# Optimization experiments

Hardware: AMD Instinct MI355X
Metric: run time of the kernel (lower is better)

## Reference

```python
import jax, jax.numpy as jnp
import numpy as np

B, NTS, NOS_F, NTS_F, H, A, HIST = 8192, 64, 7, 6, 64, 9, 2


def _lstm(x, Wih, Whh, bih, bhh):
    # x: [B, T, in] -> all hidden states [B, T, H]; torch gate order (i, f, g, o)
    xg = jnp.einsum('bti,gi->btg', x, Wih) + bih + bhh  # precompute input projection
    Hh = Whh.shape[1]

    def step(carry, xt):
        h, c = carry
        gates = xt + h @ Whh.T
        i, f, g, o = jnp.split(gates, 4, axis=-1)
        c = jax.nn.sigmoid(f) * c + jax.nn.sigmoid(i) * jnp.tanh(g)
        h = jax.nn.sigmoid(o) * jnp.tanh(c)
        return (h, c), h

    z = jnp.zeros((x.shape[0], Hh), x.dtype)
    _, hs = jax.lax.scan(step, (z, z), jnp.swapaxes(xg, 0, 1))
    return jnp.swapaxes(hs, 0, 1)


def _inner(s, WOS, bOS, Wih, Whh, bih, bhh, WTS, bTS):
    # NaN-masked ragged TS sequences + dynamic last-valid-step gather
    b = s.shape[0]
    sOS = s[:, :NOS_F]
    sTS = s[:, NOS_F:].reshape(b, -1, NTS_F)
    nan = jnp.isnan(sTS)
    n = jnp.sum(~nan[:, :, 0], axis=1)          # valid TS count per row
    h_idx = jnp.maximum(n - 1, 0)
    sTS = jnp.where(nan, 0.0, sTS)
    xOS = jax.nn.relu(sOS @ WOS.T + bOS)
    hs = _lstm(sTS, Wih, Whh, bih, bhh)
    xTS = hs[jnp.arange(b), h_idx]              # hidden state at last valid step
    xTS = jax.nn.relu(xTS @ WTS.T + bTS)
    return jnp.concatenate([xOS, xTS], axis=1)  # [B, 128]


def setup_inputs() -> dict:
    key = jax.random.key(0)
    ks = iter(jax.random.split(key, 48))

    def nanify(x, k):  # NaN-pad beyond a random valid prefix length in [1, NTS]
        lens = jax.random.randint(k, x.shape[:-2], 1, NTS + 1)
        mask = jnp.arange(NTS) < lens[..., None]
        return jnp.where(mask[..., None], x, jnp.nan)

    sTS = nanify(jax.random.normal(next(ks), (B, NTS, NTS_F)), next(ks))
    s = jnp.concatenate([jax.random.normal(next(ks), (B, NOS_F)), sTS.reshape(B, -1)], axis=1)
    shTS = nanify(jax.random.normal(next(ks), (B, HIST, NTS, NTS_F)), next(ks))
    s_hist = jnp.concatenate([jax.random.normal(next(ks), (B, HIST, NOS_F)), shTS.reshape(B, HIST, -1)], axis=2)
    hist_len = jax.random.randint(next(ks), (B,), 0, HIST + 1)
    a_hist = jnp.zeros((B, HIST, 1), jnp.float32)

    p = lambda *shape: jax.random.normal(next(ks), shape, jnp.float32) * 0.1
    inp = dict(s=s, s_hist=s_hist, a_hist=a_hist, hist_len=hist_len)
    for t in (0, 1, 2):
        inp[f'WOS{t}'] = p(H, NOS_F); inp[f'bOS{t}'] = p(H)
        inp[f'Wih{t}'] = p(4 * H, NTS_F); inp[f'Whh{t}'] = p(4 * H, H)
        inp[f'bih{t}'] = p(4 * H); inp[f'bhh{t}'] = p(4 * H)
        inp[f'WTS{t}'] = p(H, H); inp[f'bTS{t}'] = p(H)
    inp['Wiho'] = p(4 * H, 2 * H); inp['Whho'] = p(4 * H, H)
    inp['biho'] = p(4 * H); inp['bhho'] = p(4 * H)
    inp['W1'] = p(H, H); inp['b1'] = p(H)
    inp['W2'] = p(A, H); inp['b2'] = p(A)
    return inp


def reference(s, s_hist, a_hist, hist_len,
              WOS0, bOS0, Wih0, Whh0, bih0, bhh0, WTS0, bTS0,
              WOS1, bOS1, Wih1, Whh1, bih1, bhh1, WTS1, bTS1,
              WOS2, bOS2, Wih2, Whh2, bih2, bhh2, WTS2, bTS2,
              Wiho, Whho, biho, bhho, W1, b1, W2, b2):
    b = s.shape[0]
    ok2 = (hist_len >= 2)[:, None]
    # torch mutates s_hist[:,0] for hist_len<2; t1_idx==0 there, so s_t1 is also zeroed
    s_t2 = jnp.where(ok2, s_hist[:, 0, :], 0.0)
    t1_idx = jnp.maximum(hist_len - 1, 0)
    s_t1 = jnp.where(ok2, s_hist[jnp.arange(b), t1_idx, :], 0.0)

    x2 = _inner(s_t2, WOS2, bOS2, Wih2, Whh2, bih2, bhh2, WTS2, bTS2)
    x1 = _inner(s_t1, WOS1, bOS1, Wih1, Whh1, bih1, bhh1, WTS1, bTS1)
    x0 = _inner(s, WOS0, bOS0, Wih0, Whh0, bih0, bhh0, WTS0, bTS0)
    x_tilde = jnp.stack([x2, x1, x0], axis=1)  # [B, 3, 128]

    # per-batch torch.roll(shift=hist_len-2): out[t] = in[(t - shift) mod L]
    L = HIST + 1
    shift = hist_len - 2
    idx = (jnp.arange(L)[None, :] - shift[:, None]) % L
    x_tilde = jnp.take_along_axis(x_tilde, idx[:, :, None], axis=1)

    hs = _lstm(x_tilde, Wiho, Whho, biho, bhho)
    hidden = hs[jnp.arange(b), hist_len]
    x = jax.nn.relu(hidden @ W1.T + b1)
    return x @ W2.T + b2
```

## Files before the change

### kernel.cpp

```cpp
#include <hip/hip_runtime.h>
#include <hip/hip_bf16.h>

#define NB 8192
#define SROW 391

#define TW      22848
#define W_WIH   0
#define W_WHH   1536
#define W_BSUM  17920
#define W_WTS   18176
#define W_BTS   22272
#define W_WOS   22336
#define W_BOS   22784
#define W_OUT   68544
#define WO_WIHO 0
#define WO_WHHO 32768
#define WO_BSUM 49152
#define WO_W1   49408
#define WO_B1   53504
#define WO_W2   53568
#define WO_B2   54144
#define WF_TOTAL 122697

#define OFF_WHH   0
#define OFF_WIH   49152
#define OFF_WTS   73728
#define OFF_WIHO  86016
#define OFF_WHHO  118784
#define OFF_W1    135168
#define FB_TOTAL  139264

typedef unsigned short u16;
typedef __attribute__((ext_vector_type(8))) short short8;
typedef __attribute__((ext_vector_type(8))) _Float16 half8;
typedef __attribute__((ext_vector_type(4))) _Float16 half4;
typedef __attribute__((ext_vector_type(4))) float float4v;

#define MFMAH(a, b, c) __builtin_amdgcn_mfma_f32_16x16x32_f16((a), (b), (c), 0, 0, 0)

__device__ __forceinline__ float bf2f(u16 u){ return __uint_as_float(((unsigned)u) << 16); }
__device__ __forceinline__ u16 f2bf(float f){
  unsigned x = __float_as_uint(f);
  unsigned r = (x + 0x7FFFu + ((x >> 16) & 1u)) >> 16;
  return (u16)r;
}
__device__ __forceinline__ u16 f2h(float f){
  _Float16 h = (_Float16)f;
  return *(u16*)&h;
}
__device__ __forceinline__ bool isnanf32(float f){
  unsigned x = __float_as_uint(f);
  return (x & 0x7FFFFFFFu) > 0x7F800000u;
}
__device__ __forceinline__ float ldin(const void* p, size_t i, bool isbf){
  if (isbf) return bf2f(((const u16*)p)[i]);
  return ((const float*)p)[i];
}
__device__ __forceinline__ float sigm(float x){ return __fdividef(1.0f, 1.0f + __expf(-x)); }
__device__ __forceinline__ float tanh_f(float x){ return __fdividef(2.0f, 1.0f + __expf(-2.0f * x)) - 1.0f; }

__device__ __forceinline__ void lstm_cell(float gi, float gf, float gg, float go,
                                          float& cs, float& hs, bool v){
  const float ef = __expf(-gf);
  const float ei = __expf(-gi);
  const float eg = __expf(-2.0f * gg);
  const float eo = __expf(-go);
  const float A = 1.0f + ef, B = 1.0f + ei, C = 1.0f + eg;
  const float BC = B * C;
  const float R = __builtin_amdgcn_rcpf(A * BC);
  const float t = fmaf(-A, eg, A);
  const float cn = fmaf(cs, BC, t) * R;
  const float ct = fminf(fmaxf(cn, -15.0f), 15.0f);
  const float ec = __expf(-2.0f * ct);
  const float D = 1.0f + eo, E = 1.0f + ec;
  const float S = __builtin_amdgcn_rcpf(D * E);
  const float hn = (1.0f - ec) * S;
  cs = v ? cn : cs;
  hs = v ? hn : hs;
}

__device__ __forceinline__ bool detect_bf(const void* whh0){
  const u16* u = (const u16*)whh0;
  const int l = threadIdx.x & 63;
  int e = (u[2 * l] >> 7) & 0xFF;
  unsigned long long m = __ballot(e >= 100 && e <= 141);
  return __popcll(m) >= 32;
}

struct Seg { int src; int src2; int soff; int dst; int n; };
struct SegTab { Seg s[35]; };
struct PtrTab { const void* p[36]; };

__global__ __launch_bounds__(256) void kweights(PtrTab P, SegTab S, float* __restrict__ WF,
                                                const void* __restrict__ whh0, int* __restrict__ flag,
                                                int* __restrict__ ghist){
  const bool isbf = detect_bf(whh0);
  if (blockIdx.x == 0){
    if (threadIdx.x == 0) *flag = isbf ? 1 : 0;
    if (threadIdx.x < 195) ghist[threadIdx.x] = 0;
  }
  Seg sg = S.s[blockIdx.x];
  const void* a = P.p[sg.src];
  const void* b = (sg.src2 >= 0) ? P.p[sg.src2] : nullptr;
  for (int i = threadIdx.x; i < sg.n; i += 256){
    float v = ldin(a, sg.soff + i, isbf);
    if (b) v += ldin(b, sg.soff + i, isbf);
    WF[sg.dst + i] = v;
  }
}

__global__ __launch_bounds__(256) void kfrag(const float* __restrict__ WF, u16* __restrict__ FB){
  const int i = blockIdx.x * 256 + threadIdx.x;
  short8 v = {0, 0, 0, 0, 0, 0, 0, 0};
  int dst;
  if (i < 6144){
    const int lane = i & 63, f = (i >> 6) & 1, g = (i >> 7) & 3, q = (i >> 9) & 3, t = i >> 11;
    const int mrow = g * 64 + q * 16 + (lane & 15);
    const float* src = WF + t * TW + W_WHH + mrow * 64 + f * 32 + (lane >> 4) * 8;
    #pragma unroll
    for (int j = 0; j < 8; ++j) v[j] = (short)f2h(src[j]);
    dst = OFF_WHH + i * 8;
  } else if (i < 9216){
    const int k = i - 6144;
    const int lane = k & 63, g = (k >> 6) & 3, q = (k >> 8) & 3, t = k >> 10;
    if ((lane >> 4) == 0){
      const int mrow = g * 64 + q * 16 + (lane & 15);
      const float* src = WF + t * TW + W_WIH + mrow * 6;
      #pragma unroll
      for (int j = 0; j < 6; ++j) v[j] = (short)f2h(src[j]);
    }
    dst = OFF_WIH + k * 8;
  } else if (i < 10752){
    const int k = i - 9216;
    const int lane = k & 63, f = (k >> 6) & 1, q = (k >> 7) & 3, t = k >> 9;
    const int row = q * 16 + (lane & 15);
    const float* src = WF + t * TW + W_WTS + row * 64 + f * 32 + (lane >> 4) * 8;
    #pragma unroll
    for (int j = 0; j < 8; ++j) v[j] = (short)f2h(src[j]);
    dst = OFF_WTS + k * 8;
  } else if (i < 14848){
    const int k = i - 10752;
    const int lane = k & 63, f = (k >> 6) & 3, g = (k >> 8) & 3, q = (k >> 10) & 3;
    const int mrow = g * 64 + q * 16 + (lane & 15);
    const float* src = WF + W_OUT + WO_WIHO + mrow * 128 + f * 32 + (lane >> 4) * 8;
    #pragma unroll
    for (int j = 0; j < 8; ++j) v[j] = (short)f2h(src[j]);
    dst = OFF_WIHO + k * 8;
  } else if (i < 16896){
    const int k = i - 14848;
    const int lane = k & 63, f = (k >> 6) & 1, g = (k >> 7) & 3, q = (k >> 9) & 3;
    const int mrow = g * 64 + q * 16 + (lane & 15);
    const float* src = WF + W_OUT + WO_WHHO + mrow * 64 + f * 32 + (lane >> 4) * 8;
    #pragma unroll
    for (int j = 0; j < 8; ++j) v[j] = (short)f2h(src[j]);
    dst = OFF_WHHO + k * 8;
  } else {
    const int k = i - 16896;
    const int lane = k & 63, f = (k >> 6) & 1, q = (k >> 7) & 3;
    const int row = q * 16 + (lane & 15);
    const float* src = WF + W_OUT + WO_W1 + row * 64 + f * 32 + (lane >> 4) * 8;
    #pragma unroll
    for (int j = 0; j < 8; ++j) v[j] = (short)f2h(src[j]);
    dst = OFF_W1 + k * 8;
  }
  *(short8*)&FB[dst] = v;
}

__global__ __launch_bounds__(256) void kprep(const void* __restrict__ s,
                                             const void* __restrict__ sh,
                                             const int* __restrict__ hist_len,
                                             const float* __restrict__ WF,
                                             u16* __restrict__ sTx,
                                             int* __restrict__ nar,
                                             u16* __restrict__ xpartT,
                                             const int* __restrict__ flag,
                                             int* __restrict__ ghist,
                                             int* __restrict__ krank){
  __shared__ u16 stage[4][400];
  const bool isbf = (*flag != 0);
  const int t = blockIdx.y;
  const int w = threadIdx.x >> 6;
  const int l = threadIdx.x & 63;
  const int b = blockIdx.x * 4 + w;
  const int hl = hist_len[b];

  const void* base; size_t soff;
  if (t == 0){ base = s; soff = (size_t)b * SROW; }
  else {
    if (hl < 2) return;
    base = sh; soff = ((size_t)b * 2 + ((t == 1) ? 1 : 0)) * SROW;
  }

  float val[7];
  #pragma unroll
  for (int k = 0; k < 7; ++k){
    const int e = k * 64 + l;
    float v = 0.0f;
    if (e < SROW) v = isbf ? bf2f(((const u16*)base)[soff + e]) : ((const float*)base)[soff + e];
    val[k] = v;
  }
  float sOS[7];
  #pragma unroll
  for (int i = 0; i < 7; ++i) sOS[i] = __shfl(val[0], i);

  int n = 0;
  #pragma unroll
  for (int k = 0; k < 7; ++k){
    const int e = k * 64 + l;
    const bool firstf = (e >= 7) && (e < SROW) && ((e - 7) % 6 == 0);
    unsigned long long m = __ballot(firstf && !isnanf32(val[k]));
    n += __popcll(m);
  }

  #pragma unroll
  for (int k = 0; k < 7; ++k){
    const int e = k * 64 + l;
    if (e >= 7 && e < SROW) stage[w][e] = f2h(isnanf32(val[k]) ? 0.0f : val[k]);
  }

  {
    const int r = l;
    u16 v0 = stage[w][7 + 6 * r],  v1 = stage[w][8 + 6 * r],  v2 = stage[w][9 + 6 * r];
    u16 v3 = stage[w][10 + 6 * r], v4 = stage[w][11 + 6 * r], v5 = stage[w][12 + 6 * r];
    uint4 wv;
    wv.x = (uint)v0 | ((uint)v1 << 16);
    wv.y = (uint)v2 | ((uint)v3 << 16);
    wv.z = (uint)v4 | ((uint)v5 << 16);
    wv.w = 0u;
    *(uint4*)&sTx[((size_t)(t * NB + b) * 64 + r) * 8] = wv;
  }
  if (l == 0){
    nar[t * NB + b] = n;
    const int key = 64 - min(max(n, 0), 64);
    krank[t * NB + b] = atomicAdd(&ghist[t * 65 + key], 1);
  }

  const float* wos = WF + t * TW + W_WOS;
  const float* bos = WF + t * TW + W_BOS;
  float acc = bos[l];
  #pragma unroll
  for (int i = 0; i < 7; ++i) acc = fmaf(wos[l * 7 + i], sOS[i], acc);
  xpartT[((size_t)(t * NB + b)) * 128 + l] = f2h(fmaxf(acc, 0.0f));
}

__global__ __launch_bounds__(256) void kscatW(const int* __restrict__ hist_len,
                                              const int* __restrict__ nar,
                                              const int* __restrict__ ghist,
                                              const int* __restrict__ krank,
                                              int* __restrict__ idx,
                                              int* __restrict__ cnt){
  __shared__ int o[65];
  const int t = blockIdx.y;
  if (threadIdx.x == 0){
    int acc = 0;
    for (int k = 0; k < 65; ++k){ o[k] = acc; acc += ghist[t * 65 + k]; }
    if (blockIdx.x == 0) cnt[t] = acc;
  }
  __syncthreads();
  for (int i = threadIdx.x; i < 512; i += 256){
    const int b = blockIdx.x * 512 + i;
    if (t > 0 && hist_len[b] < 2) continue;
    const int key = 64 - min(max(nar[t * NB + b], 0), 64);
    idx[t * NB + o[key] + krank[t * NB + b]] = b;
  }
}

__global__ __launch_bounds__(256) void kmainM(const int* __restrict__ nar,
                                              const float* __restrict__ WF,
                                              const u16* __restrict__ FB,
                                              const u16* __restrict__ sTx,
                                              u16* __restrict__ xpartT,
                                              const int* __restrict__ idx,
                                              const int* __restrict__ cnt,
                                              u16* __restrict__ zxp){
  __shared__ u16 hH[2][16 * 72];
  __shared__ float zh[64];
  __shared__ float zg[256];
  const int t = blockIdx.y;
  const float* Wt = WF + t * TW;

  if (blockIdx.x == 0){
    if (t == 0) return;
    const int u = threadIdx.x & 63;
    const int w = threadIdx.x >> 6;
    const int row = w * 64 + u;
    const float* wr = Wt + W_WHH + row * 64;
    const float bsu = Wt[W_BSUM + row];
    if (w == 0) zh[u] = 0.0f;
    float zc = 0.0f;
    __syncthreads();
    for (int step = 0; step < 64; ++step){
      float a0 = 0.0f, a1 = 0.0f, a2 = 0.0f, a3 = 0.0f;
      #pragma unroll
      for (int k = 0; k < 64; k += 4){
        a0 = fmaf(wr[k],     zh[k],     a0);
        a1 = fmaf(wr[k + 1], zh[k + 1], a1);
        a2 = fmaf(wr[k + 2], zh[k + 2], a2);
        a3 = fmaf(wr[k + 3], zh[k + 3], a3);
      }
      zg[row] = bsu + (a0 + a1) + (a2 + a3);
      __syncthreads();
      if (w == 0){
        float gi = zg[u], gf = zg[64 + u], gg = zg[128 + u], go = zg[192 + u];
        zc = sigm(gf) * zc + sigm(gi) * tanh_f(gg);
        zh[u] = sigm(go) * tanh_f(zc);
      }
      __syncthreads();
    }
    if (w == 0){
      float acc = Wt[W_BTS + u];
      const float* wts = Wt + W_WTS + u * 64;
      for (int k = 0; k < 64; ++k) acc = fmaf(wts[k], zh[k], acc);
      zxp[(t - 1) * 128 + 64 + u] = f2h(fmaxf(acc, 0.0f));
      zxp[(t - 1) * 128 + u]      = f2h(fmaxf(Wt[W_BOS + u], 0.0f));
    }
    return;
  }

  const int c = cnt[t];
  const int bx = blockIdx.x - 1;
  if (bx * 16 >= c) return;

  const int lane = threadIdx.x & 63;
  const int q    = __builtin_amdgcn_readfirstlane((int)(threadIdx.x >> 6));
  const int nlo  = lane & 15;
  const int quad = lane >> 4;

  for (int i = threadIdx.x; i < 16 * 72; i += 256){ hH[0][i] = 0; }

  half8 aW[4][2], aX[4];
  float4v binit[4];
  #pragma unroll
  for (int g = 0; g < 4; ++g){
    #pragma unroll
    for (int f = 0; f < 2; ++f)
      aW[g][f] = *(const half8*)&FB[OFF_WHH + (((((t * 4 + q) * 4 + g) * 2 + f) * 64 + lane)) * 8];
    aX[g] = *(const half8*)&FB[OFF_WIH + ((((t * 4 + q) * 4 + g) * 64 + lane)) * 8];
    binit[g] = *(const float4v*)(Wt + W_BSUM + g * 64 + q * 16 + quad * 4);
  }

  const int pos = min(bx * 16 + nlo, c - 1);
  const int bb = idx[t * NB + pos];
  const int n_l = nar[t * NB + bb];
  const u16* sB = sTx + (size_t)(t * NB + bb) * 512;
  int nmax = n_l;
  #pragma unroll
  for (int o = 1; o < 16; o <<= 1) nmax = max(nmax, __shfl_xor(nmax, o));

  float c_st[4], h_st[4];
  #pragma unroll
  for (int r = 0; r < 4; ++r){ c_st[r] = 0.0f; h_st[r] = 0.0f; }

  half8 xcur = (half8)(_Float16)0, xnxt;
  if (lane < 16) xcur = *(const half8*)sB;

  __syncthreads();

  for (int step = 0; step < nmax; ++step){
    xnxt = (half8)(_Float16)0;
    const int ns = min(step + 1, 63);
    if (lane < 16) xnxt = *(const half8*)(sB + (size_t)ns * 8);

    const u16* rH = hH[step & 1];
    u16* wH = hH[(step + 1) & 1];

    const int hb = nlo * 72 + quad * 8;
    half8 h0 = *(const half8*)&rH[hb];
    half8 h1 = *(const half8*)&rH[hb + 32];

    float4v acc[4];
    #pragma unroll
    for (int g = 0; g < 4; ++g){
      float4v a = binit[g];
      a = MFMAH(aX[g], xcur, a);
      a = MFMAH(aW[g][0], h0, a);
      a = MFMAH(aW[g][1], h1, a);
      acc[g] = a;
    }

    const bool v = (step < n_l);
    #pragma unroll
    for (int r = 0; r < 4; ++r)
      lstm_cell(acc[0][r], acc[1][r], acc[2][r], acc[3][r], c_st[r], h_st[r], v);

    half4 hv = {(_Float16)h_st[0], (_Float16)h_st[1], (_Float16)h_st[2], (_Float16)h_st[3]};
    const int off = nlo * 72 + q * 16 + quad * 4;
    *(uint2*)&wH[off] = *(uint2*)&hv;

    xcur = xnxt;
    __syncthreads();
  }

  const u16* fH = hH[nmax & 1];
  half8 aT[2];
  #pragma unroll
  for (int f = 0; f < 2; ++f)
    aT[f] = *(const half8*)&FB[OFF_WTS + ((((t * 4 + q) * 2 + f) * 64 + lane)) * 8];
  float4v btsv = *(const float4v*)(Wt + W_BTS + q * 16 + quad * 4);
  {
    const int hb = nlo * 72 + quad * 8;
    float4v a = btsv;
    a = MFMAH(aT[0], *(const half8*)&fH[hb], a);
    a = MFMAH(aT[1], *(const half8*)&fH[hb + 32], a);
    u16 o4[4];
    #pragma unroll
    for (int r = 0; r < 4; ++r) o4[r] = f2h(fmaxf(a[r], 0.0f));
    size_t oidx = ((size_t)(t * NB + bb)) * 128 + 64 + q * 16 + quad * 4;
    uint2 wv;
    wv.x = (uint)o4[0] | ((uint)o4[1] << 16);
    wv.y = (uint)o4[2] | ((uint)o4[3] << 16);
    *(uint2*)&xpartT[oidx] = wv;
  }
}

__global__ __launch_bounds__(256) void kfinalM(const float* __restrict__ WF,
                                               const u16* __restrict__ FB,
                                               const u16* __restrict__ xpartT,
                                               const u16* __restrict__ zxp,
                                               const int* __restrict__ hist_len,
                                               void* __restrict__ out,
                                               const int* __restrict__ flag){
  __shared__ u16 hH[32 * 72];
  __shared__ float x1T[32 * 68];
  const bool isbf = (*flag != 0);
  const int b0   = blockIdx.x * 32;
  const int lane = threadIdx.x & 63;
  const int q    = __builtin_amdgcn_readfirstlane((int)(threadIdx.x >> 6));
  const int nlo  = lane & 15;
  const int quad = lane >> 4;

  for (int i = threadIdx.x; i < 32 * 72; i += 256){ hH[i] = 0; }

  const float* WO = WF + W_OUT;
  int hl2[2];
  #pragma unroll
  for (int nt = 0; nt < 2; ++nt) hl2[nt] = hist_len[b0 + nt * 16 + nlo];

  half8 aI[4][4], aH[4][2];
  float4v bi4[4];
  #pragma unroll
  for (int g = 0; g < 4; ++g){
    #pragma unroll
    for (int f = 0; f < 4; ++f)
      aI[g][f] = *(const half8*)&FB[OFF_WIHO + ((((q * 4 + g) * 4 + f) * 64 + lane)) * 8];
    #pragma unroll
    for (int f = 0; f < 2; ++f)
      aH[g][f] = *(const half8*)&FB[OFF_WHHO + ((((q * 4 + g) * 2 + f) * 64 + lane)) * 8];
    bi4[g] = *(const float4v*)(WO + WO_BSUM + g * 64 + q * 16 + quad * 4);
  }

  float c_st[2][4], h_st[2][4];
  #pragma unroll
  for (int nt = 0; nt < 2; ++nt)
    #pragma unroll
    for (int r = 0; r < 4; ++r){ c_st[nt][r] = 0.0f; h_st[nt][r] = 0.0f; }
  __syncthreads();

  for (int p = 0; p < 3; ++p){
    float4v acc[4][2];
    #pragma unroll
    for (int nt = 0; nt < 2; ++nt){
      const int bb = b0 + nt * 16 + nlo;
      const int tt = 2 - ((p - hl2[nt] + 2) % 3);
      const u16* xb = (tt > 0 && hl2[nt] < 2) ? (zxp + (tt - 1) * 128)
                                              : xpartT + ((size_t)(tt * NB + bb)) * 128;
      half8 xf[4];
      #pragma unroll
      for (int f = 0; f < 4; ++f) xf[f] = *(const half8*)(xb + f * 32 + quad * 8);
      const int hb = (nt * 16 + nlo) * 72 + quad * 8;
      half8 h0 = *(const half8*)&hH[hb];
      half8 h1 = *(const half8*)&hH[hb + 32];
      #pragma unroll
      for (int g = 0; g < 4; ++g){
        float4v a = bi4[g];
        #pragma unroll
        for (int f = 0; f < 4; ++f) a = MFMAH(aI[g][f], xf[f], a);
        a = MFMAH(aH[g][0], h0, a);
        a = MFMAH(aH[g][1], h1, a);
        acc[g][nt] = a;
      }
    }
    __syncthreads();
    #pragma unroll
    for (int nt = 0; nt < 2; ++nt){
      const bool v = (p <= hl2[nt]);
      #pragma unroll
      for (int r = 0; r < 4; ++r)
        lstm_cell(acc[0][nt][r], acc[1][nt][r], acc[2][nt][r], acc[3][nt][r],
                  c_st[nt][r], h_st[nt][r], v);
      half4 hv = {(_Float16)h_st[nt][0], (_Float16)h_st[nt][1],
                  (_Float16)h_st[nt][2], (_Float16)h_st[nt][3]};
      const int off = (nt * 16 + nlo) * 72 + q * 16 + quad * 4;
      *(uint2*)&hH[off] = *(uint2*)&hv;
    }
    __syncthreads();
  }

  half8 a1[2];
  #pragma unroll
  for (int f = 0; f < 2; ++f)
    a1[f] = *(const half8*)&FB[OFF_W1 + (((q * 2 + f) * 64 + lane)) * 8];
  float4v b1v = *(const float4v*)(WO + WO_B1 + q * 16 + quad * 4);
  #pragma unroll
  for (int nt = 0; nt < 2; ++nt){
    const int hb = (nt * 16 + nlo) * 72 + quad * 8;
    float4v a = b1v;
    a = MFMAH(a1[0], *(const half8*)&hH[hb], a);
    a = MFMAH(a1[1], *(const half8*)&hH[hb + 32], a);
    float4v rv;
    #pragma unroll
    for (int r = 0; r < 4; ++r) rv[r] = fmaxf(a[r], 0.0f);
    *(float4v*)&x1T[(nt * 16 + nlo) * 68 + q * 16 + quad * 4] = rv;
  }
  __syncthreads();

  const int bloc = threadIdx.x >> 3;
  const int r0 = threadIdx.x & 7;
  const float* w2 = WO + WO_W2;
  const float* b2 = WO + WO_B2;
  for (int r = r0; r < 9; r += 8){
    float acc = b2[r];
    const float* wr = w2 + r * 64;
    #pragma unroll
    for (int k = 0; k < 64; ++k) acc = fmaf(wr[k], x1T[bloc * 68 + k], acc);
    if (isbf) ((u16*)out)[(size_t)(b0 + bloc) * 9 + r] = f2bf(acc);
    else      ((float*)out)[(size_t)(b0 + bloc) * 9 + r] = acc;
  }
}

extern "C" void kernel_launch(void* const* d_in, const int* in_sizes, int n_in,
                              void* d_out, int out_size, void* d_ws, size_t ws_size,
                              hipStream_t stream){
  char* ws = (char*)d_ws;
  float* WF = (float*)ws;
  size_t off = ((size_t)WF_TOTAL * 4 + 255) & ~(size_t)255;
  u16* sTx = (u16*)(ws + off);    off += (size_t)3 * NB * 512 * 2;
  u16* xpartT = (u16*)(ws + off); off += (size_t)3 * NB * 128 * 2;
  int* nar = (int*)(ws + off);    off += (size_t)3 * NB * 4;
  int* flag = (int*)(ws + off);   off += 256;
  int* cnt  = (int*)(ws + off);   off += 256;
  int* ghist = (int*)(ws + off);  off += 3 * 65 * 4 + 64;
  int* idx  = (int*)(ws + off);   off += (size_t)3 * NB * 4;
  int* krank = (int*)(ws + off);  off += (size_t)3 * NB * 4;
  u16* zxp  = (u16*)(ws + off);   off += 2 * 128 * 2;
  u16* FB   = (u16*)(ws + off);   off += (size_t)FB_TOTAL * 2;

  PtrTab P;
  for (int i = 0; i < 36; ++i) P.p[i] = d_in[i];

  SegTab S;
  int si = 0;
  for (int t = 0; t < 3; ++t){
    int base = 4 + 8 * t;
    int d = t * TW;
    S.s[si++] = { base + 2, -1,       0,     d + W_WIH,         1536 };
    S.s[si++] = { base + 3, -1,       0,     d + W_WHH,         8192 };
    S.s[si++] = { base + 3, -1,       8192,  d + W_WHH + 8192,  8192 };
    S.s[si++] = { base + 4, base + 5, 0,     d + W_BSUM,        256  };
    S.s[si++] = { base + 6, -1,       0,     d + W_WTS,         4096 };
    S.s[si++] = { base + 7, -1,       0,     d + W_BTS,         64   };
    S.s[si++] = { base + 0, -1,       0,     d + W_WOS,         448  };
    S.s[si++] = { base + 1, -1,       0,     d + W_BOS,         64   };
  }
  {
    int O = W_OUT;
    for (int k = 0; k < 4; ++k)
      S.s[si++] = { 28, -1, k * 8192, O + WO_WIHO + k * 8192, 8192 };
    S.s[si++] = { 29, -1, 0,    O + WO_WHHO,        8192 };
    S.s[si++] = { 29, -1, 8192, O + WO_WHHO + 8192, 8192 };
    S.s[si++] = { 30, 31, 0,    O + WO_BSUM,        256  };
    S.s[si++] = { 32, -1, 0,    O + WO_W1,          4096 };
    S.s[si++] = { 33, -1, 0,    O + WO_B1,          64   };
    S.s[si++] = { 34, -1, 0,    O + WO_W2,          576  };
    S.s[si++] = { 35, -1, 0,    O + WO_B2,          9    };
  }

  const int* hl_ptr = (const int*)d_in[3];

  kweights<<<dim3(35), 256, 0, stream>>>(P, S, WF, d_in[7], flag, ghist);
  kfrag<<<dim3(68), 256, 0, stream>>>(WF, FB);
  kprep<<<dim3(NB / 4, 3), 256, 0, stream>>>(d_in[0], d_in[1], hl_ptr, WF, sTx, nar, xpartT, flag, ghist, krank);
  kscatW<<<dim3(16, 3), 256, 0, stream>>>(hl_ptr, nar, ghist, krank, idx, cnt);
  kmainM<<<dim3(513, 3), 256, 0, stream>>>(nar, WF, FB, sTx, xpartT, idx, cnt, zxp);
  kfinalM<<<dim3(NB / 32), 256, 0, stream>>>(WF, FB, xpartT, zxp, hl_ptr, d_out, flag);
}
```

Measured before the change: 295.4 us.

## Halve kmainM block to two waves, each computing two 16-row gate slices

The LSTM recurrence kernel now runs with 128 threads (two waves) instead of four. Each wave holds the weight fragments for two hidden-unit slices and issues twice the MFMAs per step, and the zero-input block computes two gate rows per thread. The aim is to cut the cost of the per-step __syncthreads barrier and the redundant loads of shared h fragments, and to let more blocks be resident per CU. In exchange each wave carries twice the register state, which may lower occupancy or lengthen the serial chain inside each step.

Result: slower. 315.1 us (+6.7%).

```diff
diff --git a/kernel.cpp b/kernel.cpp
--- a/kernel.cpp
+++ b/kernel.cpp
@@ -265,14 +265,14 @@
   }
 }
 
-__global__ __launch_bounds__(256) void kmainM(const int* __restrict__ nar,
-                                              const float* __restrict__ WF,
-                                              const u16* __restrict__ FB,
-                                              const u16* __restrict__ sTx,
-                                              u16* __restrict__ xpartT,
-                                              const int* __restrict__ idx,
-                                              const int* __restrict__ cnt,
-                                              u16* __restrict__ zxp){
+__global__ __launch_bounds__(128, 2) void kmainM(const int* __restrict__ nar,
+                                                 const float* __restrict__ WF,
+                                                 const u16* __restrict__ FB,
+                                                 const u16* __restrict__ sTx,
+                                                 u16* __restrict__ xpartT,
+                                                 const int* __restrict__ idx,
+                                                 const int* __restrict__ cnt,
+                                                 u16* __restrict__ zxp){
   __shared__ u16 hH[2][16 * 72];
   __shared__ float zh[64];
   __shared__ float zg[256];
@@ -283,22 +283,25 @@
     if (t == 0) return;
     const int u = threadIdx.x & 63;
     const int w = threadIdx.x >> 6;
-    const int row = w * 64 + u;
-    const float* wr = Wt + W_WHH + row * 64;
-    const float bsu = Wt[W_BSUM + row];
+    const int r0 = (int)threadIdx.x;
+    const int r1 = r0 + 128;
+    const float* wr0 = Wt + W_WHH + r0 * 64;
+    const float* wr1 = Wt + W_WHH + r1 * 64;
+    const float b0 = Wt[W_BSUM + r0];
+    const float b1 = Wt[W_BSUM + r1];
     if (w == 0) zh[u] = 0.0f;
     float zc = 0.0f;
     __syncthreads();
     for (int step = 0; step < 64; ++step){
-      float a0 = 0.0f, a1 = 0.0f, a2 = 0.0f, a3 = 0.0f;
-      #pragma unroll
-      for (int k = 0; k < 64; k += 4){
-        a0 = fmaf(wr[k],     zh[k],     a0);
-        a1 = fmaf(wr[k + 1], zh[k + 1], a1);
-        a2 = fmaf(wr[k + 2], zh[k + 2], a2);
-        a3 = fmaf(wr[k + 3], zh[k + 3], a3);
+      float a0 = 0.0f, a1 = 0.0f;
+      #pragma unroll
+      for (int k = 0; k < 64; ++k){
+        const float hv = zh[k];
+        a0 = fmaf(wr0[k], hv, a0);
+        a1 = fmaf(wr1[k], hv, a1);
       }
-      zg[row] = bsu + (a0 + a1) + (a2 + a3);
+      zg[r0] = b0 + a0;
+      zg[r1] = b1 + a1;
       __syncthreads();
       if (w == 0){
         float gi = zg[u], gf = zg[64 + u], gg = zg[128 + u], go = zg[192 + u];
@@ -322,21 +325,25 @@
   if (bx * 16 >= c) return;
 
   const int lane = threadIdx.x & 63;
-  const int q    = __builtin_amdgcn_readfirstlane((int)(threadIdx.x >> 6));
+  const int w    = __builtin_amdgcn_readfirstlane((int)(threadIdx.x >> 6));
   const int nlo  = lane & 15;
   const int quad = lane >> 4;
 
-  for (int i = threadIdx.x; i < 16 * 72; i += 256){ hH[0][i] = 0; }
-
-  half8 aW[4][2], aX[4];
-  float4v binit[4];
-  #pragma unroll
-  for (int g = 0; g < 4; ++g){
-    #pragma unroll
-    for (int f = 0; f < 2; ++f)
-      aW[g][f] = *(const half8*)&FB[OFF_WHH + (((((t * 4 + q) * 4 + g) * 2 + f) * 64 + lane)) * 8];
-    aX[g] = *(const half8*)&FB[OFF_WIH + ((((t * 4 + q) * 4 + g) * 64 + lane)) * 8];
-    binit[g] = *(const float4v*)(Wt + W_BSUM + g * 64 + q * 16 + quad * 4);
+  for (int i = threadIdx.x; i < 16 * 72; i += 128){ hH[0][i] = 0; }
+
+  half8 aW[2][4][2], aX[2][4];
+  float4v binit[2][4];
+  #pragma unroll
+  for (int s = 0; s < 2; ++s){
+    const int Q = 2 * w + s;
+    #pragma unroll
+    for (int g = 0; g < 4; ++g){
+      #pragma unroll
+      for (int f = 0; f < 2; ++f)
+        aW[s][g][f] = *(const half8*)&FB[OFF_WHH + (((((t * 4 + Q) * 4 + g) * 2 + f) * 64 + lane)) * 8];
+      aX[s][g] = *(const half8*)&FB[OFF_WIH + ((((t * 4 + Q) * 4 + g) * 64 + lane)) * 8];
+      binit[s][g] = *(const float4v*)(Wt + W_BSUM + g * 64 + Q * 16 + quad * 4);
+    }
   }
 
   const int pos = min(bx * 16 + nlo, c - 1);
@@ -347,9 +354,11 @@
   #pragma unroll
   for (int o = 1; o < 16; o <<= 1) nmax = max(nmax, __shfl_xor(nmax, o));
 
-  float c_st[4], h_st[4];
-  #pragma unroll
-  for (int r = 0; r < 4; ++r){ c_st[r] = 0.0f; h_st[r] = 0.0f; }
+  float c_st[2][4], h_st[2][4];
+  #pragma unroll
+  for (int s = 0; s < 2; ++s)
+    #pragma unroll
+    for (int r = 0; r < 4; ++r){ c_st[s][r] = 0.0f; h_st[s][r] = 0.0f; }
 
   half8 xcur = (half8)(_Float16)0, xnxt;
   if (lane < 16) xcur = *(const half8*)sB;
@@ -368,44 +377,51 @@
     half8 h0 = *(const half8*)&rH[hb];
     half8 h1 = *(const half8*)&rH[hb + 32];
 
-    float4v acc[4];
-    #pragma unroll
-    for (int g = 0; g < 4; ++g){
-      float4v a = binit[g];
-      a = MFMAH(aX[g], xcur, a);
-      a = MFMAH(aW[g][0], h0, a);
-      a = MFMAH(aW[g][1], h1, a);
-      acc[g] = a;
+    float4v acc[2][4];
+    #pragma unroll
+    for (int s = 0; s < 2; ++s)
+      #pragma unroll
+      for (int g = 0; g < 4; ++g){
+        float4v a = binit[s][g];
+        a = MFMAH(aX[s][g], xcur, a);
+        a = MFMAH(aW[s][g][0], h0, a);
+        a = MFMAH(aW[s][g][1], h1, a);
+        acc[s][g] = a;
+      }
+
+    const bool v = (step < n_l);
+    #pragma unroll
+    for (int s = 0; s < 2; ++s){
+      #pragma unroll
+      for (int r = 0; r < 4; ++r)
+        lstm_cell(acc[s][0][r], acc[s][1][r], acc[s][2][r], acc[s][3][r],
+                  c_st[s][r], h_st[s][r], v);
+      half4 hv = {(_Float16)h_st[s][0], (_Float16)h_st[s][1],
+                  (_Float16)h_st[s][2], (_Float16)h_st[s][3]};
+      const int off = nlo * 72 + (2 * w + s) * 16 + quad * 4;
+      *(uint2*)&wH[off] = *(uint2*)&hv;
     }
-
-    const bool v = (step < n_l);
-    #pragma unroll
-    for (int r = 0; r < 4; ++r)
-      lstm_cell(acc[0][r], acc[1][r], acc[2][r], acc[3][r], c_st[r], h_st[r], v);
-
-    half4 hv = {(_Float16)h_st[0], (_Float16)h_st[1], (_Float16)h_st[2], (_Float16)h_st[3]};
-    const int off = nlo * 72 + q * 16 + quad * 4;
-    *(uint2*)&wH[off] = *(uint2*)&hv;
 
     xcur = xnxt;
     __syncthreads();
   }
 
   const u16* fH = hH[nmax & 1];
-  half8 aT[2];
-  #pragma unroll
-  for (int f = 0; f < 2; ++f)
-    aT[f] = *(const half8*)&FB[OFF_WTS + ((((t * 4 + q) * 2 + f) * 64 + lane)) * 8];
-  float4v btsv = *(const float4v*)(Wt + W_BTS + q * 16 + quad * 4);
-  {
-    const int hb = nlo * 72 + quad * 8;
-    float4v a = btsv;
-    a = MFMAH(aT[0], *(const half8*)&fH[hb], a);
-    a = MFMAH(aT[1], *(const half8*)&fH[hb + 32], a);
+  const int hb = nlo * 72 + quad * 8;
+  const half8 fh0 = *(const half8*)&fH[hb];
+  const half8 fh1 = *(const half8*)&fH[hb + 32];
+  #pragma unroll
+  for (int s = 0; s < 2; ++s){
+    const int Q = 2 * w + s;
+    half8 aT0 = *(const half8*)&FB[OFF_WTS + ((((t * 4 + Q) * 2 + 0) * 64 + lane)) * 8];
+    half8 aT1 = *(const half8*)&FB[OFF_WTS + ((((t * 4 + Q) * 2 + 1) * 64 + lane)) * 8];
+    float4v a = *(const float4v*)(Wt + W_BTS + Q * 16 + quad * 4);
+    a = MFMAH(aT0, fh0, a);
+    a = MFMAH(aT1, fh1, a);
     u16 o4[4];
     #pragma unroll
     for (int r = 0; r < 4; ++r) o4[r] = f2h(fmaxf(a[r], 0.0f));
-    size_t oidx = ((size_t)(t * NB + bb)) * 128 + 64 + q * 16 + quad * 4;
+    size_t oidx = ((size_t)(t * NB + bb)) * 128 + 64 + Q * 16 + quad * 4;
     uint2 wv;
     wv.x = (uint)o4[0] | ((uint)o4[1] << 16);
     wv.y = (uint)o4[2] | ((uint)o4[3] << 16);
@@ -581,6 +597,6 @@
   kfrag<<<dim3(68), 256, 0, stream>>>(WF, FB);
   kprep<<<dim3(NB / 4, 3), 256, 0, stream>>>(d_in[0], d_in[1], hl_ptr, WF, sTx, nar, xpartT, flag, ghist, krank);
   kscatW<<<dim3(16, 3), 256, 0, stream>>>(hl_ptr, nar, ghist, krank, idx, cnt);
-  kmainM<<<dim3(513, 3), 256, 0, stream>>>(nar, WF, FB, sTx, xpartT, idx, cnt, zxp);
+  kmainM<<<dim3(513, 3), 128, 0, stream>>>(nar, WF, FB, sTx, xpartT, idx, cnt, zxp);
   kfinalM<<<dim3(NB / 32), 256, 0, stream>>>(WF, FB, xpartT, zxp, hl_ptr, d_out, flag);
 }
```

## Halve batch tile in final LSTM kernel and raise MFMA priority in main loop

Applied to the files above, without the earlier changes.

The final output-LSTM kernel now handles 16 batch rows per block instead of 32, doubling the grid to 512 blocks and dropping the inner two-tile loop. This spreads the work across more CUs and shortens each block's serial path, at the cost of loading the weight fragments twice as often overall. The main recurrent kernel also wraps its MFMA gate computation in s_setprio(1)/s_setprio(0) so those instructions get scheduling priority over other waves.

Result: no change. 294.2 us (-0.4%).

```diff
diff --git a/kernel.cpp b/kernel.cpp
--- a/kernel.cpp
+++ b/kernel.cpp
@@ -368,6 +368,7 @@
     half8 h0 = *(const half8*)&rH[hb];
     half8 h1 = *(const half8*)&rH[hb + 32];
 
+    __builtin_amdgcn_s_setprio(1);
     float4v acc[4];
     #pragma unroll
     for (int g = 0; g < 4; ++g){
@@ -377,6 +378,7 @@
       a = MFMAH(aW[g][1], h1, a);
       acc[g] = a;
     }
+    __builtin_amdgcn_s_setprio(0);
 
     const bool v = (step < n_l);
     #pragma unroll
@@ -420,21 +422,19 @@
                                                const int* __restrict__ hist_len,
                                                void* __restrict__ out,
                                                const int* __restrict__ flag){
-  __shared__ u16 hH[32 * 72];
-  __shared__ float x1T[32 * 68];
+  __shared__ u16 hH[16 * 72];
+  __shared__ float x1T[16 * 68];
   const bool isbf = (*flag != 0);
-  const int b0   = blockIdx.x * 32;
+  const int b0   = blockIdx.x * 16;
   const int lane = threadIdx.x & 63;
   const int q    = __builtin_amdgcn_readfirstlane((int)(threadIdx.x >> 6));
   const int nlo  = lane & 15;
   const int quad = lane >> 4;
 
-  for (int i = threadIdx.x; i < 32 * 72; i += 256){ hH[i] = 0; }
+  for (int i = threadIdx.x; i < 16 * 72; i += 256){ hH[i] = 0; }
 
   const float* WO = WF + W_OUT;
-  int hl2[2];
-  #pragma unroll
-  for (int nt = 0; nt < 2; ++nt) hl2[nt] = hist_len[b0 + nt * 16 + nlo];
+  const int hl = hist_len[b0 + nlo];
 
   half8 aI[4][4], aH[4][2];
   float4v bi4[4];
@@ -449,48 +449,41 @@
     bi4[g] = *(const float4v*)(WO + WO_BSUM + g * 64 + q * 16 + quad * 4);
   }
 
-  float c_st[2][4], h_st[2][4];
-  #pragma unroll
-  for (int nt = 0; nt < 2; ++nt)
-    #pragma unroll
-    for (int r = 0; r < 4; ++r){ c_st[nt][r] = 0.0f; h_st[nt][r] = 0.0f; }
+  float c_st[4], h_st[4];
+  #pragma unroll
+  for (int r = 0; r < 4; ++r){ c_st[r] = 0.0f; h_st[r] = 0.0f; }
   __syncthreads();
 
   for (int p = 0; p < 3; ++p){
-    float4v acc[4][2];
-    #pragma unroll
-    for (int nt = 0; nt < 2; ++nt){
-      const int bb = b0 + nt * 16 + nlo;
-      const int tt = 2 - ((p - hl2[nt] + 2) % 3);
-      const u16* xb = (tt > 0 && hl2[nt] < 2) ? (zxp + (tt - 1) * 128)
-                                              : xpartT + ((size_t)(tt * NB + bb)) * 128;
-      half8 xf[4];
+    const int bb = b0 + nlo;
+    const int tt = 2 - ((p - hl + 2) % 3);
+    const u16* xb = (tt > 0 && hl < 2) ? (zxp + (tt - 1) * 128)
+                                       : xpartT + ((size_t)(tt * NB + bb)) * 128;
+    half8 xf[4];
+    #pragma unroll
+    for (int f = 0; f < 4; ++f) xf[f] = *(const half8*)(xb + f * 32 + quad * 8);
+    const int hb = nlo * 72 + quad * 8;
+    half8 h0 = *(const half8*)&hH[hb];
+    half8 h1 = *(const half8*)&hH[hb + 32];
+    float4v acc[4];
+    #pragma unroll
+    for (int g = 0; g < 4; ++g){
+      float4v a = bi4[g];
       #pragma unroll
-      for (int f = 0; f < 4; ++f) xf[f] = *(const half8*)(xb + f * 32 + quad * 8);
-      const int hb = (nt * 16 + nlo) * 72 + quad * 8;
-      half8 h0 = *(const half8*)&hH[hb];
-      half8 h1 = *(const half8*)&hH[hb + 32];
-      #pragma unroll
-      for (int g = 0; g < 4; ++g){
-        float4v a = bi4[g];
-        #pragma unroll
-        for (int f = 0; f < 4; ++f) a = MFMAH(aI[g][f], xf[f], a);
-        a = MFMAH(aH[g][0], h0, a);
-        a = MFMAH(aH[g][1], h1, a);
-        acc[g][nt] = a;
-      }
+      for (int f = 0; f < 4; ++f) a = MFMAH(aI[g][f], xf[f], a);
+      a = MFMAH(aH[g][0], h0, a);
+      a = MFMAH(aH[g][1], h1, a);
+      acc[g] = a;
     }
     __syncthreads();
-    #pragma unroll
-    for (int nt = 0; nt < 2; ++nt){
-      const bool v = (p <= hl2[nt]);
+    {
+      const bool v = (p <= hl);
       #pragma unroll
       for (int r = 0; r < 4; ++r)
-        lstm_cell(acc[0][nt][r], acc[1][nt][r], acc[2][nt][r], acc[3][nt][r],
-                  c_st[nt][r], h_st[nt][r], v);
-      half4 hv = {(_Float16)h_st[nt][0], (_Float16)h_st[nt][1],
-                  (_Float16)h_st[nt][2], (_Float16)h_st[nt][3]};
-      const int off = (nt * 16 + nlo) * 72 + q * 16 + quad * 4;
+        lstm_cell(acc[0][r], acc[1][r], acc[2][r], acc[3][r], c_st[r], h_st[r], v);
+      half4 hv = {(_Float16)h_st[0], (_Float16)h_st[1],
+                  (_Float16)h_st[2], (_Float16)h_st[3]};
+      const int off = nlo * 72 + q * 16 + quad * 4;
       *(uint2*)&hH[off] = *(uint2*)&hv;
     }
     __syncthreads();
@@ -501,30 +494,29 @@
   for (int f = 0; f < 2; ++f)
     a1[f] = *(const half8*)&FB[OFF_W1 + (((q * 2 + f) * 64 + lane)) * 8];
   float4v b1v = *(const float4v*)(WO + WO_B1 + q * 16 + quad * 4);
-  #pragma unroll
-  for (int nt = 0; nt < 2; ++nt){
-    const int hb = (nt * 16 + nlo) * 72 + quad * 8;
+  {
+    const int hb = nlo * 72 + quad * 8;
     float4v a = b1v;
     a = MFMAH(a1[0], *(const half8*)&hH[hb], a);
     a = MFMAH(a1[1], *(const half8*)&hH[hb + 32], a);
     float4v rv;
     #pragma unroll
     for (int r = 0; r < 4; ++r) rv[r] = fmaxf(a[r], 0.0f);
-    *(float4v*)&x1T[(nt * 16 + nlo) * 68 + q * 16 + quad * 4] = rv;
+    *(float4v*)&x1T[nlo * 68 + q * 16 + quad * 4] = rv;
   }
   __syncthreads();
 
-  const int bloc = threadIdx.x >> 3;
-  const int r0 = threadIdx.x & 7;
+  const int bloc = threadIdx.x >> 4;
+  const int r0 = threadIdx.x & 15;
   const float* w2 = WO + WO_W2;
   const float* b2 = WO + WO_B2;
-  for (int r = r0; r < 9; r += 8){
-    float acc = b2[r];
-    const float* wr = w2 + r * 64;
+  if (r0 < 9){
+    float acc = b2[r0];
+    const float* wr = w2 + r0 * 64;
     #pragma unroll
     for (int k = 0; k < 64; ++k) acc = fmaf(wr[k], x1T[bloc * 68 + k], acc);
-    if (isbf) ((u16*)out)[(size_t)(b0 + bloc) * 9 + r] = f2bf(acc);
-    else      ((float*)out)[(size_t)(b0 + bloc) * 9 + r] = acc;
+    if (isbf) ((u16*)out)[(size_t)(b0 + bloc) * 9 + r0] = f2bf(acc);
+    else      ((float*)out)[(size_t)(b0 + bloc) * 9 + r0] = acc;
   }
 }
 
@@ -582,5 +574,5 @@
   kprep<<<dim3(NB / 4, 3), 256, 0, stream>>>(d_in[0], d_in[1], hl_ptr, WF, sTx, nar, xpartT, flag, ghist, krank);
   kscatW<<<dim3(16, 3), 256, 0, stream>>>(hl_ptr, nar, ghist, krank, idx, cnt);
   kmainM<<<dim3(513, 3), 256, 0, stream>>>(nar, WF, FB, sTx, xpartT, idx, cnt, zxp);
-  kfinalM<<<dim3(NB / 32), 256, 0, stream>>>(WF, FB, xpartT, zxp, hl_ptr, d_out, flag);
-}
+  kfinalM<<<dim3(NB / 16), 256, 0, stream>>>(WF, FB, xpartT, zxp, hl_ptr, d_out, flag);
+}
```
